# Kernel optimization log

Measured on AMD Instinct MI355X. Metric: run time of the kernel, lower is better.

## Reference

```python
import jax, jax.numpy as jnp
import numpy as np


def setup_inputs() -> dict:
    B, S, DK, DV, H = 2, 2048, 1024, 1024, 16
    ks = jax.random.split(jax.random.key(0), 7)
    keys = jax.random.normal(ks[0], (B, S, DK), jnp.float32)
    queries = jax.random.normal(ks[1], (B, S, DK), jnp.float32)
    values = jax.random.normal(ks[2], (B, S, DV), jnp.float32)
    # per-head projection weights, stored as [H, in, out] (torch Linear uses W.T; math-equivalent)
    WQ = jax.random.normal(ks[3], (H, DK, DK // H), jnp.float32) / np.sqrt(DK).astype(np.float32)
    WK = jax.random.normal(ks[4], (H, DK, DK // H), jnp.float32) / np.sqrt(DK).astype(np.float32)
    WV = jax.random.normal(ks[5], (H, DV, DV // H), jnp.float32) / np.sqrt(DV).astype(np.float32)
    WO = jax.random.normal(ks[6], (DV, DV), jnp.float32) / np.sqrt(DV).astype(np.float32)
    return {"keys": keys, "queries": queries, "values": values,
            "WQ": WQ, "WK": WK, "WV": WV, "WO": WO, "masking": 1}


def reference(keys, queries, values, WQ, WK, WV, WO, masking):
    B, Sq, _ = queries.shape
    Sk = keys.shape[1]
    # batched per-head projections (original loops over heads in Python)
    Q = jnp.einsum('bqd,hde->bhqe', queries, WQ)   # [B,H,Sq,dh]
    K = jnp.einsum('bkd,hde->bhke', keys, WK)      # [B,H,Sk,dh]
    V = jnp.einsum('bkd,hde->bhke', values, WV)    # [B,H,Sk,dvh]
    q_idx = jnp.arange(Sq)[:, None]
    k_idx = jnp.arange(Sk)[None, :]
    causal = k_idx <= q_idx
    # NOTE: original never applies the slope m; bias = (i - j) for i<=j else 0, same for all heads
    bias = jnp.where(causal, (k_idx - q_idx).astype(jnp.float32), 0.0)
    scale = np.float32(1.0 / np.sqrt(Sk))  # original divides by sqrt(keys.shape[1])
    y = (jnp.einsum('bhqe,bhke->bhqk', Q, K) + bias) * scale
    if masking:
        y = jnp.where(causal, y, -jnp.inf)
    # original: F.softmax(y, 1) on [B,Sq,Sk] -> softmax over the QUERY axis
    z = jax.nn.softmax(y, axis=2)
    out = jnp.einsum('bhqk,bhke->bhqe', z, V)      # [B,H,Sq,dvh]
    out = out.transpose(0, 2, 1, 3).reshape(B, Sq, -1)  # concat heads on last dim
    return out @ WO
```

## Files before the change

### kernel.cpp

```cpp
#include <hip/hip_runtime.h>
#include <math.h>

#define SEQ    2048
#define DMODEL 1024
#define NH     16
#define DH     64
#define NB     2
#define BHN    (NB*NH)

static constexpr float SCALE  = 0.02209708691207961f;
static constexpr float SCALE2 = 0.02209708691207961f * 1.4426950408889634f;

typedef __attribute__((ext_vector_type(8))) short short8;
typedef __attribute__((ext_vector_type(4))) short short4v;
typedef __attribute__((ext_vector_type(4))) float f32x4;

__device__ __forceinline__ short f2bf(float f) {
    union { float f; unsigned u; } v; v.f = f;
    unsigned r = (v.u + 0x7FFFu + ((v.u >> 16) & 1u)) >> 16;
    return (short)r;
}

__device__ __forceinline__ unsigned pack_bf2(float a, float b) {
    union { float f; unsigned u; } ua, ub; ua.f = a; ub.f = b;
    return __builtin_amdgcn_perm(ub.u + 0x8000u, ua.u + 0x8000u, 0x07060302u);
}

__device__ __forceinline__ float bf2f(short s) {
    union { unsigned u; float f; } v; v.u = ((unsigned)(unsigned short)s) << 16;
    return v.f;
}

__device__ __forceinline__ void load16_lds(const short* g, short* l) {
    __builtin_amdgcn_global_load_lds(
        (const __attribute__((address_space(1))) unsigned int*)g,
        (__attribute__((address_space(3))) unsigned int*)l,
        16, 0, 0);
}

__device__ __forceinline__ void stage_rows(const short* g, short* s, int t, int ldg, int nIter) {
    int wave = t >> 6, lane = t & 63;
    #pragma unroll
    for (int i = 0; i < 4; ++i) {
        if (i >= nIter) break;
        int E   = i * 2048 + wave * 512 + lane * 8;
        int row = E >> 6;
        int blk = (lane & 7) ^ (row & 7);
        load16_lds(g + (size_t)row * ldg + blk * 8, s + i * 2048 + wave * 512);
    }
}

__device__ __forceinline__ short8 frag_sw(const short* s, int rowbase, int ks, int lane) {
    int m   = rowbase + (lane & 15);
    int q   = lane >> 4;
    int blk = (ks * 4 + q) ^ (m & 7);
    return *(const short8*)(s + m * 64 + blk * 8);
}

__device__ __forceinline__ void swizzle_tile(int x, int y, int& tile, int& bh) {
    int r = y >> 3;
    bh = (y & 7) * 4 + r;
    int xs = (r & 2) ? ((x + 16) & 31) : x;
    tile = (r & 1) ? (31 - xs) : xs;
}

__global__ __launch_bounds__(256) void convert_x(
    const float* __restrict__ q, const float* __restrict__ k, const float* __restrict__ v,
    short* __restrict__ Xq, short* __restrict__ Xk, short* __restrict__ Xv)
{
    const int z = blockIdx.z;
    const float* src = (z == 0) ? q : (z == 1) ? k : v;
    short* dst = (z == 0) ? Xq : (z == 1) ? Xk : Xv;
    size_t idx = ((size_t)blockIdx.x * 256 + threadIdx.x) * 8;
    float4 a = *(const float4*)(src + idx);
    float4 b = *(const float4*)(src + idx + 4);
    short8 o;
    o[0] = f2bf(a.x); o[1] = f2bf(a.y); o[2] = f2bf(a.z); o[3] = f2bf(a.w);
    o[4] = f2bf(b.x); o[5] = f2bf(b.y); o[6] = f2bf(b.z); o[7] = f2bf(b.w);
    *(short8*)(dst + idx) = o;
}

__global__ __launch_bounds__(256) void convert_w(
    const float* __restrict__ WQ, const float* __restrict__ WK,
    const float* __restrict__ WV, const float* __restrict__ WO,
    short* __restrict__ WQt, short* __restrict__ WKt,
    short* __restrict__ WVt, short* __restrict__ WOt)
{
    const int z = blockIdx.z;
    const int k0 = blockIdx.x * 64;
    const int ny = blockIdx.y;
    const float* W = (z == 0) ? WQ : (z == 1) ? WK : (z == 2) ? WV : WO;
    short* Wt = (z == 0) ? WQt : (z == 1) ? WKt : (z == 2) ? WVt : WOt;

    __shared__ float Ts[64][68];
    const int t = threadIdx.x;
    const int tr = t >> 4, tc4 = (t & 15) * 4;

    #pragma unroll
    for (int i = 0; i < 4; ++i) {
        int row = tr + i * 16;
        float4 v;
        if (z < 3) v = *(const float4*)(W + (size_t)ny * DMODEL * DH + (size_t)(k0 + row) * DH + tc4);
        else       v = *(const float4*)(W + (size_t)(k0 + row) * DMODEL + ny * 64 + tc4);
        Ts[tc4 + 0][row] = v.x; Ts[tc4 + 1][row] = v.y;
        Ts[tc4 + 2][row] = v.z; Ts[tc4 + 3][row] = v.w;
    }
    __syncthreads();
    #pragma unroll
    for (int i = 0; i < 4; ++i) {
        int nl = tr + i * 16;
        short4v o;
        o[0] = f2bf(Ts[nl][tc4 + 0]); o[1] = f2bf(Ts[nl][tc4 + 1]);
        o[2] = f2bf(Ts[nl][tc4 + 2]); o[3] = f2bf(Ts[nl][tc4 + 3]);
        *(short4v*)(Wt + (size_t)(ny * 64 + nl) * DMODEL + k0 + tc4) = o;
    }
}

__global__ __launch_bounds__(256) void gemm_nt(
    const short* __restrict__ A0, const short* __restrict__ A1, const short* __restrict__ A2,
    const short* __restrict__ B0, const short* __restrict__ B1, const short* __restrict__ B2,
    short* __restrict__ Y0, short* __restrict__ Y1, short* __restrict__ Y2,
    float* __restrict__ outF, int phase)
{
    const int z = blockIdx.z;
    const short* X  = (phase == 1) ? A0 : (z == 0) ? A0 : (z == 1) ? A1 : A2;
    const short* Wt = (phase == 1) ? B0 : (z == 0) ? B0 : (z == 1) ? B1 : B2;
    short* Y        = (z == 0) ? Y0 : (z == 1) ? Y1 : Y2;
    const bool vOrient = (phase == 0) && (z == 2);

    const int n0 = blockIdx.x * 128;
    const int m0 = blockIdx.y * 128;

    __shared__ short As[128 * 64];
    __shared__ short Bs[128 * 64];

    const int t = threadIdx.x;
    const int wave = t >> 6, lane = t & 63;
    const int wrow = (wave >> 1) * 64, wcol = (wave & 1) * 64;
    const int quad = lane >> 4, l15 = lane & 15;

    f32x4 acc[4][4];
    #pragma unroll
    for (int i = 0; i < 4; ++i)
        #pragma unroll
        for (int j = 0; j < 4; ++j)
            acc[i][j] = (f32x4)0.f;

    for (int k0 = 0; k0 < DMODEL; k0 += 64) {
        __syncthreads();
        stage_rows(X  + (size_t)m0 * DMODEL + k0, As, t, DMODEL, 4);
        stage_rows(Wt + (size_t)n0 * DMODEL + k0, Bs, t, DMODEL, 4);
        __syncthreads();
        if (!vOrient) {
            #pragma unroll
            for (int ks = 0; ks < 2; ++ks) {
                short8 xf[4], wf[4];
                #pragma unroll
                for (int i = 0; i < 4; ++i) xf[i] = frag_sw(As, wrow + i * 16, ks, lane);
                #pragma unroll
                for (int i = 0; i < 4; ++i) wf[i] = frag_sw(Bs, wcol + i * 16, ks, lane);
                #pragma unroll
                for (int a = 0; a < 4; ++a)
                    #pragma unroll
                    for (int b = 0; b < 4; ++b)
                        acc[a][b] = __builtin_amdgcn_mfma_f32_16x16x32_bf16(
                            wf[a], xf[b], acc[a][b], 0, 0, 0);
            }
        } else {
            #pragma unroll
            for (int ks = 0; ks < 2; ++ks) {
                short8 xf[4], wf[4];
                #pragma unroll
                for (int i = 0; i < 4; ++i) xf[i] = frag_sw(As, wrow + i * 16, ks, lane);
                #pragma unroll
                for (int i = 0; i < 4; ++i) wf[i] = frag_sw(Bs, wcol + i * 16, ks, lane);
                #pragma unroll
                for (int a = 0; a < 4; ++a)
                    #pragma unroll
                    for (int b = 0; b < 4; ++b)
                        acc[a][b] = __builtin_amdgcn_mfma_f32_16x16x32_bf16(
                            xf[a], wf[b], acc[a][b], 0, 0, 0);
            }
        }
    }

    if (vOrient) {
        #pragma unroll
        for (int a = 0; a < 4; ++a) {
            #pragma unroll
            for (int b = 0; b < 4; ++b) {
                int m = m0 + wrow + a * 16 + quad * 4;
                int n = n0 + wcol + b * 16 + l15;
                int bb = m >> 11, s = m & 2047, h = n >> 6, e = n & 63;
                short4v o;
                #pragma unroll
                for (int i = 0; i < 4; ++i) o[i] = f2bf(acc[a][b][i]);
                *(short4v*)(Y + ((size_t)((bb * NH + h) * DH + e)) * SEQ + s) = o;
            }
        }
    } else if (phase == 1) {
        #pragma unroll
        for (int a = 0; a < 4; ++a) {
            #pragma unroll
            for (int b = 0; b < 4; ++b) {
                int n = n0 + wcol + a * 16 + quad * 4;
                int m = m0 + wrow + b * 16 + l15;
                float4 o = make_float4(acc[a][b][0], acc[a][b][1], acc[a][b][2], acc[a][b][3]);
                *(float4*)(outF + (size_t)m * DMODEL + n) = o;
            }
        }
    } else {
        #pragma unroll
        for (int a = 0; a < 4; ++a) {
            #pragma unroll
            for (int b = 0; b < 4; ++b) {
                int n = n0 + wcol + a * 16 + quad * 4;
                int m = m0 + wrow + b * 16 + l15;
                int bb = m >> 11, s = m & 2047, h = n >> 6, e = n & 63;
                short4v o;
                #pragma unroll
                for (int i = 0; i < 4; ++i) o[i] = f2bf(acc[a][b][i]);
                *(short4v*)(Y + ((size_t)((bb * NH + h) * SEQ + s)) * DH + e) = o;
            }
        }
    }
}

template<int MODE>
__device__ __forceinline__ void stats_tile_w(
    const short* Qbuf, const short8 Kf[2], const float bias[4][4],
    float dsum[4], int lane, int wave16)
{
    const int quad = lane >> 4, l15 = lane & 15;
    f32x4 acc[4];
    #pragma unroll
    for (int nt = 0; nt < 4; ++nt) acc[nt] = (f32x4)0.f;
    #pragma unroll
    for (int ks = 0; ks < 2; ++ks) {
        #pragma unroll
        for (int nt = 0; nt < 4; ++nt)
            acc[nt] = __builtin_amdgcn_mfma_f32_16x16x32_bf16(
                Kf[ks], frag_sw(Qbuf, nt * 16, ks, lane), acc[nt], 0, 0, 0);
    }
    #pragma unroll
    for (int nt = 0; nt < 4; ++nt) {
        #pragma unroll
        for (int i = 0; i < 4; ++i) {
            float bi = bias[nt][i];
            float v = (MODE == 2) ? fmaf(acc[nt][i], SCALE2, fminf(bi, 0.f))
                                  : fmaf(acc[nt][i], SCALE2, bi);
            float e = exp2f(v);
            if (MODE == 1)
                e = ((wave16 + quad * 4 + i) <= (nt * 16 + l15)) ? e : 0.f;
            dsum[i] += e;
        }
    }
}

__global__ __launch_bounds__(256) void stats_mfma(
    const short* __restrict__ Qg, const short* __restrict__ Kg,
    short* __restrict__ Vt, const int* __restrict__ mask_p)
{
    int kt, bh;
    swizzle_tile(blockIdx.x, blockIdx.y, kt, bh);
    const int k0 = kt * 64;
    const int masking = mask_p[0];

    __shared__ short Ks[64 * 64];
    __shared__ short Qs[2][64 * 64];
    __shared__ float rDs[64];

    const int t = threadIdx.x;
    const int wave = t >> 6, lane = t & 63;
    const int quad = lane >> 4, l15 = lane & 15;

    const int q0s = masking ? k0 : 0;
    stage_rows(Kg + ((size_t)bh * SEQ + k0) * DH, Ks, t, DH, 2);
    stage_rows(Qg + ((size_t)bh * SEQ + q0s) * DH, Qs[0], t, DH, 2);
    __syncthreads();

    short8 Kf[2];
    Kf[0] = frag_sw(Ks, wave * 16, 0, lane);
    Kf[1] = frag_sw(Ks, wave * 16, 1, lane);

    float bias[4][4];
    #pragma unroll
    for (int nt = 0; nt < 4; ++nt)
        #pragma unroll
        for (int i = 0; i < 4; ++i)
            bias[nt][i] = SCALE2 * (float)((k0 + wave * 16 + quad * 4 + i)
                                         - (q0s + nt * 16 + l15));

    float dsum[4] = {0.f, 0.f, 0.f, 0.f};
    const int nIter = (SEQ - q0s) / 64;
    for (int it = 0; it < nIter; ++it) {
        const int cur = it & 1;
        if (it > 0) __syncthreads();
        if (it + 1 < nIter)
            stage_rows(Qg + ((size_t)bh * SEQ + q0s + (it + 1) * 64) * DH, Qs[1 - cur], t, DH, 2);
        if (!masking)      stats_tile_w<2>(Qs[cur], Kf, bias, dsum, lane, wave * 16);
        else if (it == 0)  stats_tile_w<1>(Qs[cur], Kf, bias, dsum, lane, wave * 16);
        else               stats_tile_w<0>(Qs[cur], Kf, bias, dsum, lane, wave * 16);
        #pragma unroll
        for (int nt = 0; nt < 4; ++nt)
            #pragma unroll
            for (int i = 0; i < 4; ++i)
                bias[nt][i] -= 64.f * SCALE2;
    }

    #pragma unroll
    for (int i = 0; i < 4; ++i) {
        float d = dsum[i];
        #pragma unroll
        for (int mm = 1; mm < 16; mm <<= 1) d += __shfl_xor(d, mm);
        dsum[i] = d;
    }
    if (l15 == 0) {
        const int kloc = wave * 16 + quad * 4;
        float4 o = make_float4(1.f / dsum[0], 1.f / dsum[1], 1.f / dsum[2], 1.f / dsum[3]);
        *(float4*)&rDs[kloc] = o;
    }
    __syncthreads();

    short* vp = Vt + (size_t)bh * DH * SEQ + k0;
    #pragma unroll
    for (int c = t; c < 512; c += 256) {
        int e = c >> 3, sc = (c & 7) * 8;
        short* p = vp + (size_t)e * SEQ + sc;
        short8 v = *(short8*)p;
        union { unsigned u[4]; short8 s8; } o;
        #pragma unroll
        for (int j = 0; j < 4; ++j)
            o.u[j] = pack_bf2(bf2f(v[2 * j]) * rDs[sc + 2 * j],
                              bf2f(v[2 * j + 1]) * rDs[sc + 2 * j + 1]);
        *(short8*)p = o.s8;
    }
}

template<int MODE>
__device__ __forceinline__ void attn_tile(
    const short* Kbuf, const short* Vbuf, short* Pw,
    const short8 Qf[2], const float bias[4][4], f32x4 oacc[4],
    int lane, int quad, int l15, int qloc)
{
    f32x4 sacc[4];
    #pragma unroll
    for (int mt = 0; mt < 4; ++mt) sacc[mt] = (f32x4)0.f;
    #pragma unroll
    for (int ks = 0; ks < 2; ++ks) {
        #pragma unroll
        for (int mt = 0; mt < 4; ++mt)
            sacc[mt] = __builtin_amdgcn_mfma_f32_16x16x32_bf16(
                frag_sw(Kbuf, mt * 16, ks, lane), Qf[ks], sacc[mt], 0, 0, 0);
    }
    __asm__ volatile("" ::: "memory");
    #pragma unroll
    for (int mt = 0; mt < 4; ++mt) {
        float p[4];
        #pragma unroll
        for (int i = 0; i < 4; ++i) {
            float bi = bias[mt][i];
            float v = (MODE == 2) ? fmaf(sacc[mt][i], SCALE2, fminf(bi, 0.f))
                                  : fmaf(sacc[mt][i], SCALE2, bi);
            float e = exp2f(v);
            if (MODE == 1)
                e = ((mt * 16 + quad * 4 + i) <= qloc) ? e : 0.f;
            p[i] = e;
        }
        int blk = (2 * mt + (quad >> 1)) ^ (l15 & 7);
        *(uint2*)(Pw + l15 * 64 + blk * 8 + (quad & 1) * 4) =
            make_uint2(pack_bf2(p[0], p[1]), pack_bf2(p[2], p[3]));
    }
    __asm__ volatile("" ::: "memory");
    #pragma unroll
    for (int ks = 0; ks < 2; ++ks) {
        short8 pf = *(const short8*)(Pw + l15 * 64 + (((ks * 4 + quad) ^ (l15 & 7)) * 8));
        #pragma unroll
        for (int mt = 0; mt < 4; ++mt)
            oacc[mt] = __builtin_amdgcn_mfma_f32_16x16x32_bf16(
                frag_sw(Vbuf, mt * 16, ks, lane), pf, oacc[mt], 0, 0, 0);
    }
}

__global__ __launch_bounds__(256) void attn_mfma(
    const short* __restrict__ Qg, const short* __restrict__ Kg, const short* __restrict__ Vt,
    short* __restrict__ attnb, const int* __restrict__ mask_p)
{
    int qt, bh;
    swizzle_tile(blockIdx.x, blockIdx.y, qt, bh);
    const int b = bh / NH, h = bh % NH;
    const int q0 = qt * 64;
    const int masking = mask_p[0];

    __shared__ short Qs[64 * 64];
    __shared__ short Ks[64 * 64];
    __shared__ short Vts[64 * 64];

    const int t = threadIdx.x;
    const int wave = t >> 6, lane = t & 63;
    const int quad = lane >> 4, l15 = lane & 15;
    short* Pw = Qs + wave * 1024;
    const int qloc = wave * 16 + l15;

    stage_rows(Qg + ((size_t)bh * SEQ + q0) * DH, Qs, t, DH, 2);
    __syncthreads();

    short8 Qf[2];
    Qf[0] = frag_sw(Qs, wave * 16, 0, lane);
    Qf[1] = frag_sw(Qs, wave * 16, 1, lane);

    float bias[4][4];
    #pragma unroll
    for (int mt = 0; mt < 4; ++mt)
        #pragma unroll
        for (int i = 0; i < 4; ++i)
            bias[mt][i] = SCALE2 * (float)((mt * 16 + quad * 4 + i)
                                         - (q0 + qloc));

    f32x4 oacc[4];
    #pragma unroll
    for (int mt = 0; mt < 4; ++mt) oacc[mt] = (f32x4)0.f;

    const int nIter = masking ? (qt + 1) : (SEQ / 64);
    for (int it = 0; it < nIter; ++it) {
        __syncthreads();
        stage_rows(Kg + ((size_t)bh * SEQ + it * 64) * DH, Ks, t, DH, 2);
        stage_rows(Vt + (size_t)bh * DH * SEQ + it * 64, Vts, t, SEQ, 2);
        __syncthreads();
        if (!masking)       attn_tile<2>(Ks, Vts, Pw, Qf, bias, oacc, lane, quad, l15, qloc);
        else if (it == qt)  attn_tile<1>(Ks, Vts, Pw, Qf, bias, oacc, lane, quad, l15, qloc);
        else                attn_tile<0>(Ks, Vts, Pw, Qf, bias, oacc, lane, quad, l15, qloc);
        #pragma unroll
        for (int mt = 0; mt < 4; ++mt)
            #pragma unroll
            for (int i = 0; i < 4; ++i)
                bias[mt][i] += 64.f * SCALE2;
    }

    #pragma unroll
    for (int mt = 0; mt < 4; ++mt) {
        int e = mt * 16 + quad * 4;
        int q = q0 + wave * 16 + l15;
        short4v o;
        #pragma unroll
        for (int i = 0; i < 4; ++i) o[i] = f2bf(oacc[mt][i]);
        *(short4v*)(attnb + ((size_t)(b * SEQ + q)) * DMODEL + h * DH + e) = o;
    }
}

extern "C" void kernel_launch(void* const* d_in, const int* in_sizes, int n_in,
                              void* d_out, int out_size, void* d_ws, size_t ws_size,
                              hipStream_t stream) {
    const float* keys    = (const float*)d_in[0];
    const float* queries = (const float*)d_in[1];
    const float* values  = (const float*)d_in[2];
    const float* WQ      = (const float*)d_in[3];
    const float* WK      = (const float*)d_in[4];
    const float* WV      = (const float*)d_in[5];
    const float* WO      = (const float*)d_in[6];
    const int*   mask_p  = (const int*)d_in[7];
    float* out = (float*)d_out;

    const size_t nX = (size_t)NB * SEQ * DMODEL;
    const size_t nW = (size_t)DMODEL * DMODEL;
    const size_t nQ = (size_t)BHN * SEQ * DH;

    short* ws = (short*)d_ws;
    short* Xq    = ws;
    short* Xk    = Xq + nX;
    short* Xv    = Xk + nX;
    short* WQt   = Xv + nX;
    short* WKt   = WQt + nW;
    short* WVt   = WKt + nW;
    short* WOt   = WVt + nW;
    short* Qg    = WOt + nW;
    short* Kg    = Qg + nQ;
    short* Vtg   = Kg + nQ;
    short* attnb = Vtg + nQ;

    convert_x<<<dim3(2048, 1, 3), dim3(256), 0, stream>>>(queries, keys, values, Xq, Xk, Xv);
    convert_w<<<dim3(16, 16, 4), dim3(256), 0, stream>>>(WQ, WK, WV, WO, WQt, WKt, WVt, WOt);
    gemm_nt<<<dim3(8, 32, 3), dim3(256), 0, stream>>>(
        Xq, Xk, Xv, WQt, WKt, WVt, Qg, Kg, Vtg, nullptr, 0);
    stats_mfma<<<dim3(32, 32), dim3(256), 0, stream>>>(Qg, Kg, Vtg, mask_p);
    attn_mfma<<<dim3(32, 32), dim3(256), 0, stream>>>(Qg, Kg, Vtg, attnb, mask_p);
    gemm_nt<<<dim3(8, 32, 1), dim3(256), 0, stream>>>(
        attnb, nullptr, nullptr, WOt, nullptr, nullptr, nullptr, nullptr, nullptr, out, 1);
}
```

Baseline: 275.5 us.

## Enlarge stats and attention tiles to 128 rows and double-buffer K/V staging

The column-stats kernel now processes 128 key rows per block, and the attention kernel processes 128 query rows per block, with each wave handling two 16-row groups. Each staged Q or K/V tile is therefore reused across twice as many rows, and the K fragments are hoisted out of the per-group loop. The attention kernel also double-buffers its K/V shared-memory tiles, so the next tile loads while the current one computes, replacing the two barriers per iteration with one. In exchange, grids are halved, which gives fewer blocks and coarser causal load imbalance, and register and LDS pressure per block goes up, with launch bounds set to keep occupancy.

```diff
diff --git a/kernel.cpp b/kernel.cpp
--- a/kernel.cpp
+++ b/kernel.cpp
@@ -8,7 +8,6 @@
 #define NB     2
 #define BHN    (NB*NH)
 
-static constexpr float SCALE  = 0.02209708691207961f;
 static constexpr float SCALE2 = 0.02209708691207961f * 1.4426950408889634f;
 
 typedef __attribute__((ext_vector_type(8))) short short8;
@@ -57,11 +56,11 @@
     return *(const short8*)(s + m * 64 + blk * 8);
 }
 
-__device__ __forceinline__ void swizzle_tile(int x, int y, int& tile, int& bh) {
+__device__ __forceinline__ void swizzle16(int x, int y, int& tile, int& bh) {
     int r = y >> 3;
     bh = (y & 7) * 4 + r;
-    int xs = (r & 2) ? ((x + 16) & 31) : x;
-    tile = (r & 1) ? (31 - xs) : xs;
+    int xs = (r & 2) ? ((x + 8) & 15) : x;
+    tile = (r & 1) ? (15 - xs) : xs;
 }
 
 __global__ __launch_bounds__(256) void convert_x(
@@ -226,62 +225,76 @@
     }
 }
 
-template<int MODE>
-__device__ __forceinline__ void stats_tile_w(
-    const short* Qbuf, const short8 Kf[2], const float bias[4][4],
-    float dsum[4], int lane, int wave16)
+template<int M0, int M1>
+__device__ __forceinline__ void stats_tile128(
+    const short* Qbuf, const short8 Kf[2][2], const float bias[4][4],
+    float dsum[2][4], int lane, int wave16)
 {
     const int quad = lane >> 4, l15 = lane & 15;
-    f32x4 acc[4];
-    #pragma unroll
-    for (int nt = 0; nt < 4; ++nt) acc[nt] = (f32x4)0.f;
-    #pragma unroll
-    for (int ks = 0; ks < 2; ++ks) {
+    const float C64 = 64.f * SCALE2;
+    short8 qf[2][4];
+    #pragma unroll
+    for (int ks = 0; ks < 2; ++ks)
         #pragma unroll
         for (int nt = 0; nt < 4; ++nt)
-            acc[nt] = __builtin_amdgcn_mfma_f32_16x16x32_bf16(
-                Kf[ks], frag_sw(Qbuf, nt * 16, ks, lane), acc[nt], 0, 0, 0);
-    }
-    #pragma unroll
-    for (int nt = 0; nt < 4; ++nt) {
-        #pragma unroll
-        for (int i = 0; i < 4; ++i) {
-            float bi = bias[nt][i];
-            float v = (MODE == 2) ? fmaf(acc[nt][i], SCALE2, fminf(bi, 0.f))
-                                  : fmaf(acc[nt][i], SCALE2, bi);
-            float e = exp2f(v);
-            if (MODE == 1)
-                e = ((wave16 + quad * 4 + i) <= (nt * 16 + l15)) ? e : 0.f;
-            dsum[i] += e;
-        }
-    }
-}
-
-__global__ __launch_bounds__(256) void stats_mfma(
+            qf[ks][nt] = frag_sw(Qbuf, nt * 16, ks, lane);
+    #pragma unroll
+    for (int kg = 0; kg < 2; ++kg) {
+        const int MODE = kg ? M1 : M0;
+        if (MODE == 3) continue;
+        f32x4 acc[4];
+        #pragma unroll
+        for (int nt = 0; nt < 4; ++nt) acc[nt] = (f32x4)0.f;
+        #pragma unroll
+        for (int ks = 0; ks < 2; ++ks)
+            #pragma unroll
+            for (int nt = 0; nt < 4; ++nt)
+                acc[nt] = __builtin_amdgcn_mfma_f32_16x16x32_bf16(
+                    Kf[kg][ks], qf[ks][nt], acc[nt], 0, 0, 0);
+        #pragma unroll
+        for (int nt = 0; nt < 4; ++nt) {
+            #pragma unroll
+            for (int i = 0; i < 4; ++i) {
+                float bi = bias[nt][i] + (kg ? C64 : 0.f);
+                float v = (MODE == 2) ? fmaf(acc[nt][i], SCALE2, fminf(bi, 0.f))
+                                      : fmaf(acc[nt][i], SCALE2, bi);
+                float e = exp2f(v);
+                if (MODE == 1)
+                    e = ((wave16 + quad * 4 + i) <= (nt * 16 + l15)) ? e : 0.f;
+                dsum[kg][i] += e;
+            }
+        }
+    }
+}
+
+__global__ __launch_bounds__(256, 4) void stats_mfma(
     const short* __restrict__ Qg, const short* __restrict__ Kg,
     short* __restrict__ Vt, const int* __restrict__ mask_p)
 {
     int kt, bh;
-    swizzle_tile(blockIdx.x, blockIdx.y, kt, bh);
-    const int k0 = kt * 64;
+    swizzle16(blockIdx.x, blockIdx.y, kt, bh);
+    const int k0 = kt * 128;
     const int masking = mask_p[0];
 
-    __shared__ short Ks[64 * 64];
+    __shared__ short Ks[128 * 64];
     __shared__ short Qs[2][64 * 64];
-    __shared__ float rDs[64];
+    __shared__ float rDs[128];
 
     const int t = threadIdx.x;
     const int wave = t >> 6, lane = t & 63;
     const int quad = lane >> 4, l15 = lane & 15;
 
     const int q0s = masking ? k0 : 0;
-    stage_rows(Kg + ((size_t)bh * SEQ + k0) * DH, Ks, t, DH, 2);
+    stage_rows(Kg + ((size_t)bh * SEQ + k0) * DH, Ks, t, DH, 4);
     stage_rows(Qg + ((size_t)bh * SEQ + q0s) * DH, Qs[0], t, DH, 2);
     __syncthreads();
 
-    short8 Kf[2];
-    Kf[0] = frag_sw(Ks, wave * 16, 0, lane);
-    Kf[1] = frag_sw(Ks, wave * 16, 1, lane);
+    short8 Kf[2][2];
+    #pragma unroll
+    for (int kg = 0; kg < 2; ++kg)
+        #pragma unroll
+        for (int ks = 0; ks < 2; ++ks)
+            Kf[kg][ks] = frag_sw(Ks, kg * 64 + wave * 16, ks, lane);
 
     float bias[4][4];
     #pragma unroll
@@ -291,16 +304,17 @@
             bias[nt][i] = SCALE2 * (float)((k0 + wave * 16 + quad * 4 + i)
                                          - (q0s + nt * 16 + l15));
 
-    float dsum[4] = {0.f, 0.f, 0.f, 0.f};
+    float dsum[2][4] = {{0.f,0.f,0.f,0.f},{0.f,0.f,0.f,0.f}};
     const int nIter = (SEQ - q0s) / 64;
     for (int it = 0; it < nIter; ++it) {
         const int cur = it & 1;
         if (it > 0) __syncthreads();
         if (it + 1 < nIter)
             stage_rows(Qg + ((size_t)bh * SEQ + q0s + (it + 1) * 64) * DH, Qs[1 - cur], t, DH, 2);
-        if (!masking)      stats_tile_w<2>(Qs[cur], Kf, bias, dsum, lane, wave * 16);
-        else if (it == 0)  stats_tile_w<1>(Qs[cur], Kf, bias, dsum, lane, wave * 16);
-        else               stats_tile_w<0>(Qs[cur], Kf, bias, dsum, lane, wave * 16);
+        if (!masking)      stats_tile128<2,2>(Qs[cur], Kf, bias, dsum, lane, wave * 16);
+        else if (it == 0)  stats_tile128<1,3>(Qs[cur], Kf, bias, dsum, lane, wave * 16);
+        else if (it == 1)  stats_tile128<0,1>(Qs[cur], Kf, bias, dsum, lane, wave * 16);
+        else               stats_tile128<0,0>(Qs[cur], Kf, bias, dsum, lane, wave * 16);
         #pragma unroll
         for (int nt = 0; nt < 4; ++nt)
             #pragma unroll
@@ -309,23 +323,27 @@
     }
 
     #pragma unroll
-    for (int i = 0; i < 4; ++i) {
-        float d = dsum[i];
-        #pragma unroll
-        for (int mm = 1; mm < 16; mm <<= 1) d += __shfl_xor(d, mm);
-        dsum[i] = d;
-    }
-    if (l15 == 0) {
-        const int kloc = wave * 16 + quad * 4;
-        float4 o = make_float4(1.f / dsum[0], 1.f / dsum[1], 1.f / dsum[2], 1.f / dsum[3]);
-        *(float4*)&rDs[kloc] = o;
+    for (int kg = 0; kg < 2; ++kg) {
+        #pragma unroll
+        for (int i = 0; i < 4; ++i) {
+            float d = dsum[kg][i];
+            #pragma unroll
+            for (int mm = 1; mm < 16; mm <<= 1) d += __shfl_xor(d, mm);
+            dsum[kg][i] = d;
+        }
+        if (l15 == 0) {
+            const int kloc = kg * 64 + wave * 16 + quad * 4;
+            float4 o = make_float4(1.f / dsum[kg][0], 1.f / dsum[kg][1],
+                                   1.f / dsum[kg][2], 1.f / dsum[kg][3]);
+            *(float4*)&rDs[kloc] = o;
+        }
     }
     __syncthreads();
 
     short* vp = Vt + (size_t)bh * DH * SEQ + k0;
     #pragma unroll
-    for (int c = t; c < 512; c += 256) {
-        int e = c >> 3, sc = (c & 7) * 8;
+    for (int c = t; c < 1024; c += 256) {
+        int e = c >> 4, sc = (c & 15) * 8;
         short* p = vp + (size_t)e * SEQ + sc;
         short8 v = *(short8*)p;
         union { unsigned u[4]; short8 s8; } o;
@@ -338,76 +356,97 @@
 }
 
 template<int MODE>
-__device__ __forceinline__ void attn_tile(
+__device__ __forceinline__ void attn_tile128(
     const short* Kbuf, const short* Vbuf, short* Pw,
-    const short8 Qf[2], const float bias[4][4], f32x4 oacc[4],
-    int lane, int quad, int l15, int qloc)
-{
-    f32x4 sacc[4];
-    #pragma unroll
-    for (int mt = 0; mt < 4; ++mt) sacc[mt] = (f32x4)0.f;
+    const short8 Qf[2][2], const float bias[4][4], f32x4 oacc[2][4],
+    int lane, int quad, int l15, int qo0)
+{
+    const float C16 = 16.f * SCALE2;
+    short8 Kf2[2][4];
+    #pragma unroll
+    for (int ks = 0; ks < 2; ++ks)
+        #pragma unroll
+        for (int mt = 0; mt < 4; ++mt)
+            Kf2[ks][mt] = frag_sw(Kbuf, mt * 16, ks, lane);
+    __asm__ volatile("" ::: "memory");
+    #pragma unroll
+    for (int qg = 0; qg < 2; ++qg) {
+        f32x4 sacc[4];
+        #pragma unroll
+        for (int mt = 0; mt < 4; ++mt) sacc[mt] = (f32x4)0.f;
+        #pragma unroll
+        for (int ks = 0; ks < 2; ++ks)
+            #pragma unroll
+            for (int mt = 0; mt < 4; ++mt)
+                sacc[mt] = __builtin_amdgcn_mfma_f32_16x16x32_bf16(
+                    Kf2[ks][mt], Qf[qg][ks], sacc[mt], 0, 0, 0);
+        const int rq = qg * 16 + l15;
+        #pragma unroll
+        for (int mt = 0; mt < 4; ++mt) {
+            float p[4];
+            #pragma unroll
+            for (int i = 0; i < 4; ++i) {
+                float bi = bias[mt][i] - (qg ? C16 : 0.f);
+                float v = (MODE == 2) ? fmaf(sacc[mt][i], SCALE2, fminf(bi, 0.f))
+                                      : fmaf(sacc[mt][i], SCALE2, bi);
+                float e = exp2f(v);
+                if (MODE == 1)
+                    e = ((mt * 16 + quad * 4 + i) <= (qo0 + qg * 16)) ? e : 0.f;
+                p[i] = e;
+            }
+            int blk = (2 * mt + (quad >> 1)) ^ (l15 & 7);
+            *(uint2*)(Pw + rq * 64 + blk * 8 + (quad & 1) * 4) =
+                make_uint2(pack_bf2(p[0], p[1]), pack_bf2(p[2], p[3]));
+        }
+    }
+    __asm__ volatile("" ::: "memory");
     #pragma unroll
     for (int ks = 0; ks < 2; ++ks) {
-        #pragma unroll
-        for (int mt = 0; mt < 4; ++mt)
-            sacc[mt] = __builtin_amdgcn_mfma_f32_16x16x32_bf16(
-                frag_sw(Kbuf, mt * 16, ks, lane), Qf[ks], sacc[mt], 0, 0, 0);
-    }
-    __asm__ volatile("" ::: "memory");
-    #pragma unroll
-    for (int mt = 0; mt < 4; ++mt) {
-        float p[4];
-        #pragma unroll
-        for (int i = 0; i < 4; ++i) {
-            float bi = bias[mt][i];
-            float v = (MODE == 2) ? fmaf(sacc[mt][i], SCALE2, fminf(bi, 0.f))
-                                  : fmaf(sacc[mt][i], SCALE2, bi);
-            float e = exp2f(v);
-            if (MODE == 1)
-                e = ((mt * 16 + quad * 4 + i) <= qloc) ? e : 0.f;
-            p[i] = e;
-        }
-        int blk = (2 * mt + (quad >> 1)) ^ (l15 & 7);
-        *(uint2*)(Pw + l15 * 64 + blk * 8 + (quad & 1) * 4) =
-            make_uint2(pack_bf2(p[0], p[1]), pack_bf2(p[2], p[3]));
-    }
-    __asm__ volatile("" ::: "memory");
-    #pragma unroll
-    for (int ks = 0; ks < 2; ++ks) {
-        short8 pf = *(const short8*)(Pw + l15 * 64 + (((ks * 4 + quad) ^ (l15 & 7)) * 8));
-        #pragma unroll
-        for (int mt = 0; mt < 4; ++mt)
-            oacc[mt] = __builtin_amdgcn_mfma_f32_16x16x32_bf16(
-                frag_sw(Vbuf, mt * 16, ks, lane), pf, oacc[mt], 0, 0, 0);
-    }
-}
-
-__global__ __launch_bounds__(256) void attn_mfma(
+        short8 vf[4];
+        #pragma unroll
+        for (int mt = 0; mt < 4; ++mt) vf[mt] = frag_sw(Vbuf, mt * 16, ks, lane);
+        #pragma unroll
+        for (int qg = 0; qg < 2; ++qg) {
+            const int rq = qg * 16 + l15;
+            short8 pf = *(const short8*)(Pw + rq * 64 + (((ks * 4 + quad) ^ (l15 & 7)) * 8));
+            #pragma unroll
+            for (int mt = 0; mt < 4; ++mt)
+                oacc[qg][mt] = __builtin_amdgcn_mfma_f32_16x16x32_bf16(
+                    vf[mt], pf, oacc[qg][mt], 0, 0, 0);
+        }
+    }
+}
+
+__global__ __launch_bounds__(256, 3) void attn_mfma(
     const short* __restrict__ Qg, const short* __restrict__ Kg, const short* __restrict__ Vt,
     short* __restrict__ attnb, const int* __restrict__ mask_p)
 {
     int qt, bh;
-    swizzle_tile(blockIdx.x, blockIdx.y, qt, bh);
+    swizzle16(blockIdx.x, blockIdx.y, qt, bh);
     const int b = bh / NH, h = bh % NH;
-    const int q0 = qt * 64;
+    const int q0 = qt * 128;
     const int masking = mask_p[0];
 
-    __shared__ short Qs[64 * 64];
-    __shared__ short Ks[64 * 64];
-    __shared__ short Vts[64 * 64];
+    __shared__ short Qs[128 * 64];
+    __shared__ short Ks[2][64 * 64];
+    __shared__ short Vts[2][64 * 64];
 
     const int t = threadIdx.x;
     const int wave = t >> 6, lane = t & 63;
     const int quad = lane >> 4, l15 = lane & 15;
-    short* Pw = Qs + wave * 1024;
-    const int qloc = wave * 16 + l15;
-
-    stage_rows(Qg + ((size_t)bh * SEQ + q0) * DH, Qs, t, DH, 2);
+    short* Pw = Qs + wave * 2048;
+
+    stage_rows(Qg + ((size_t)bh * SEQ + q0) * DH, Qs, t, DH, 4);
+    stage_rows(Kg + (size_t)bh * SEQ * DH, Ks[0], t, DH, 2);
+    stage_rows(Vt + (size_t)bh * DH * SEQ, Vts[0], t, SEQ, 2);
     __syncthreads();
 
-    short8 Qf[2];
-    Qf[0] = frag_sw(Qs, wave * 16, 0, lane);
-    Qf[1] = frag_sw(Qs, wave * 16, 1, lane);
+    short8 Qf[2][2];
+    #pragma unroll
+    for (int qg = 0; qg < 2; ++qg)
+        #pragma unroll
+        for (int ks = 0; ks < 2; ++ks)
+            Qf[qg][ks] = frag_sw(Qs, wave * 32 + qg * 16, ks, lane);
 
     float bias[4][4];
     #pragma unroll
@@ -415,21 +454,30 @@
         #pragma unroll
         for (int i = 0; i < 4; ++i)
             bias[mt][i] = SCALE2 * (float)((mt * 16 + quad * 4 + i)
-                                         - (q0 + qloc));
-
-    f32x4 oacc[4];
-    #pragma unroll
-    for (int mt = 0; mt < 4; ++mt) oacc[mt] = (f32x4)0.f;
-
-    const int nIter = masking ? (qt + 1) : (SEQ / 64);
+                                         - (q0 + wave * 32 + l15));
+
+    f32x4 oacc[2][4];
+    #pragma unroll
+    for (int qg = 0; qg < 2; ++qg)
+        #pragma unroll
+        for (int mt = 0; mt < 4; ++mt) oacc[qg][mt] = (f32x4)0.f;
+
+    const int nIter = masking ? (2 * qt + 2) : (SEQ / 64);
     for (int it = 0; it < nIter; ++it) {
-        __syncthreads();
-        stage_rows(Kg + ((size_t)bh * SEQ + it * 64) * DH, Ks, t, DH, 2);
-        stage_rows(Vt + (size_t)bh * DH * SEQ + it * 64, Vts, t, SEQ, 2);
-        __syncthreads();
-        if (!masking)       attn_tile<2>(Ks, Vts, Pw, Qf, bias, oacc, lane, quad, l15, qloc);
-        else if (it == qt)  attn_tile<1>(Ks, Vts, Pw, Qf, bias, oacc, lane, quad, l15, qloc);
-        else                attn_tile<0>(Ks, Vts, Pw, Qf, bias, oacc, lane, quad, l15, qloc);
+        const int cur = it & 1;
+        if (it > 0) __syncthreads();
+        if (it + 1 < nIter) {
+            const int k0n = (it + 1) * 64;
+            stage_rows(Kg + ((size_t)bh * SEQ + k0n) * DH, Ks[1 - cur], t, DH, 2);
+            stage_rows(Vt + (size_t)bh * DH * SEQ + k0n, Vts[1 - cur], t, SEQ, 2);
+        }
+        const int qo0 = (q0 - it * 64) + wave * 32 + l15;
+        if (!masking)
+            attn_tile128<2>(Ks[cur], Vts[cur], Pw, Qf, bias, oacc, lane, quad, l15, qo0);
+        else if (it >= nIter - 2)
+            attn_tile128<1>(Ks[cur], Vts[cur], Pw, Qf, bias, oacc, lane, quad, l15, qo0);
+        else
+            attn_tile128<0>(Ks[cur], Vts[cur], Pw, Qf, bias, oacc, lane, quad, l15, qo0);
         #pragma unroll
         for (int mt = 0; mt < 4; ++mt)
             #pragma unroll
@@ -438,13 +486,16 @@
     }
 
     #pragma unroll
-    for (int mt = 0; mt < 4; ++mt) {
-        int e = mt * 16 + quad * 4;
-        int q = q0 + wave * 16 + l15;
-        short4v o;
-        #pragma unroll
-        for (int i = 0; i < 4; ++i) o[i] = f2bf(oacc[mt][i]);
-        *(short4v*)(attnb + ((size_t)(b * SEQ + q)) * DMODEL + h * DH + e) = o;
+    for (int qg = 0; qg < 2; ++qg) {
+        int q = q0 + wave * 32 + qg * 16 + l15;
+        #pragma unroll
+        for (int mt = 0; mt < 4; ++mt) {
+            int e = mt * 16 + quad * 4;
+            short4v o;
+            #pragma unroll
+            for (int i = 0; i < 4; ++i) o[i] = f2bf(oacc[qg][mt][i]);
+            *(short4v*)(attnb + ((size_t)(b * SEQ + q)) * DMODEL + h * DH + e) = o;
+        }
     }
 }
 
@@ -482,8 +533,8 @@
     convert_w<<<dim3(16, 16, 4), dim3(256), 0, stream>>>(WQ, WK, WV, WO, WQt, WKt, WVt, WOt);
     gemm_nt<<<dim3(8, 32, 3), dim3(256), 0, stream>>>(
         Xq, Xk, Xv, WQt, WKt, WVt, Qg, Kg, Vtg, nullptr, 0);
-    stats_mfma<<<dim3(32, 32), dim3(256), 0, stream>>>(Qg, Kg, Vtg, mask_p);
-    attn_mfma<<<dim3(32, 32), dim3(256), 0, stream>>>(Qg, Kg, Vtg, attnb, mask_p);
+    stats_mfma<<<dim3(16, 32), dim3(256), 0, stream>>>(Qg, Kg, Vtg, mask_p);
+    attn_mfma<<<dim3(16, 32), dim3(256), 0, stream>>>(Qg, Kg, Vtg, attnb, mask_p);
     gemm_nt<<<dim3(8, 32, 1), dim3(256), 0, stream>>>(
         attnb, nullptr, nullptr, WOt, nullptr, nullptr, nullptr, nullptr, nullptr, out, 1);
 }
```

Result: slower. 307.4 us (+11.6%).
